# Kernel optimization log

Measured on AMD Instinct MI355X. Metric: run time of the kernel, lower is better.

The kernel has to match this reference:

```python
import jax, jax.numpy as jnp
import numpy as np

B, N1, N2, E = 128, 128, 384, 1024
N = N1 + N2
D_IN, D_FC = 64, 128
NUM_HEADS = 8.0  # args.num_att_heads
THETA = 1.0      # args.al_scale


def setup_inputs() -> dict:
    key = jax.random.key(0)
    ks = jax.random.split(key, 14)
    c_hs = jax.random.normal(ks[0], (B, N, D_IN), jnp.float32)
    attention = jax.random.uniform(ks[1], (B, N1, N2), jnp.float32)
    coords = jax.random.normal(ks[2], (B, N, 3), jnp.float32)
    upd_coords = coords + 0.1 * jax.random.normal(ks[3], (B, N, 3), jnp.float32)
    c_valid = jnp.ones((B, N), jnp.float32)
    nm = (jax.random.uniform(ks[4], (B, N1)) < 0.7).astype(jnp.float32)
    mapping = (jax.random.uniform(ks[5], (B, N, N)) < 0.05).astype(jnp.float32)
    samelb = jnp.maximum(mapping, (jax.random.uniform(ks[6], (B, N, N)) < 0.1).astype(jnp.float32))
    edge_index = jax.random.randint(ks[7], (B, E, 2), 0, N1, jnp.int32)
    W0 = jax.random.normal(ks[8], (D_IN, D_FC), jnp.float32) * 0.05
    b0 = jnp.zeros((D_FC,), jnp.float32)
    W1 = jax.random.normal(ks[9], (D_FC, D_FC), jnp.float32) * 0.05
    b1 = jnp.zeros((D_FC,), jnp.float32)
    W2 = jax.random.normal(ks[10], (D_FC, D_FC), jnp.float32) * 0.05
    b2 = jnp.zeros((D_FC,), jnp.float32)
    W3 = jax.random.normal(ks[11], (D_FC, 1), jnp.float32) * 0.05
    b3 = jnp.zeros((1,), jnp.float32)
    return dict(c_hs=c_hs, attention=attention, coords=coords, upd_coords=upd_coords,
                c_valid=c_valid, nm=nm, mapping=mapping, samelb=samelb,
                edge_index=edge_index, W0=W0, b0=b0, W1=W1, b1=b1, W2=W2, b2=b2, W3=W3, b3=b3)


def _kabsch(P, Q, m):
    # P, Q: [N1, 3], m: [N1] 0/1 non-modified mask
    Pm = P.mean(0)
    Qm = Q.mean(0)
    h = (P - Pm).T @ (Q - Qm) / NUM_HEADS  # [3,3]
    u, s, vt = jnp.linalg.svd(h)
    d = jnp.sign(jnp.linalg.det(h))
    corr = jnp.diag(jnp.concatenate([jnp.ones((2,), h.dtype), d[None].astype(h.dtype)]))
    r = u @ corr @ vt
    trans = Qm - r @ Pm
    Pp = P @ r.T + trans
    mk = (m > 0.5).astype(P.dtype)[:, None]
    cnt = jnp.maximum(mk.sum() * 3.0, 1.0)
    new_rmsd = (mk * (Pp - Q) ** 2).sum() / cnt        # mse over selected rows
    cen = ((Pp.mean(0) - Qm) ** 2).mean()              # centroid mse
    return new_rmsd, cen


def reference(c_hs, attention, coords, upd_coords, c_valid, nm, mapping, samelb,
              edge_index, W0, b0, W1, b1, W2, b2, W3, b3):
    # --- segment-sum pooling (sum_var_parts) + divide by n1, then FC head ---
    pooled = (c_hs * c_valid[..., None]).sum(axis=1) / float(N1)   # [B, D_IN]
    h = jax.nn.relu(pooled @ W0 + b0)
    h = jax.nn.relu(h @ W1 + b1)
    h = jax.nn.relu(h @ W2 + b2)
    scores = jax.nn.sigmoid(h @ W3 + b3).reshape(-1)               # [B]

    # --- cal_atten_batch + F.normalize(dim=1) ---
    atten = jnp.zeros((B, N, N), c_hs.dtype)
    atten = atten.at[:, :N1, N1:].set(attention)
    atten = atten.at[:, N1:, :N1].set(jnp.swapaxes(attention, 1, 2))
    nrm = jnp.sqrt((atten ** 2).sum(axis=1, keepdims=True))
    atten = atten / jnp.maximum(nrm, 1e-12)

    # --- cal_attn_loss ---
    top = jnp.where(mapping == 1.0, jnp.exp(-(atten * mapping)), 0.0).sum(axis=(1, 2))
    topabot = jnp.where(samelb == 1.0, jnp.exp(-(atten * samelb)), 0.0).sum(axis=(1, 2))
    attn_loss = (top / (topabot - top + 1.0)).sum() * THETA / float(B)

    # --- cal_rmsd_loss: straight-through one-hot mapping + Kabsch/SVD ---
    PP = upd_coords[:, :N1]   # subgraph updated coords
    QQ = coords[:, N1:]       # target graph original coords
    oh = jax.nn.one_hot(jnp.argmax(attention, axis=-1), N2, dtype=attention.dtype)
    st = oh + attention - jax.lax.stop_gradient(attention)         # straight-through
    Qsel = jnp.einsum('bij,bjd->bid', st, QQ)                      # [B, N1, 3]
    new_rmsd, cen = jax.vmap(_kabsch)(PP, Qsel, nm)
    rmsd_loss = new_rmsd.mean()
    centroid_loss = cen.mean()

    # --- cal_pairdst_loss over subgraph edges ---
    sub_c = coords[:, :N1]
    sub_u = upd_coords[:, :N1]
    bidx = jnp.arange(B)[:, None]
    d0 = jnp.sqrt(((sub_c[bidx, edge_index[..., 0]] - sub_c[bidx, edge_index[..., 1]]) ** 2).sum(-1) + 1e-12)
    d1 = jnp.sqrt(((sub_u[bidx, edge_index[..., 0]] - sub_u[bidx, edge_index[..., 1]]) ** 2).sum(-1) + 1e-12)
    pairdst_loss = jnp.abs((d1 - d0).sum(axis=-1)).mean()

    return scores, attn_loss, rmsd_loss, pairdst_loss, centroid_loss
```

## Files before the change

### kernel.cpp

```cpp
#include <hip/hip_runtime.h>
#include <math.h>

#define B_   128
#define N1_  128
#define N2_  384
#define N_   512
#define E_   1024
#define DIN  64
#define DFC  128

#define ACC_TOP  0
#define ACC_BOT  128
#define POOL_OFF 256
#define RNI_OFF  (POOL_OFF + B_*DIN)
#define CNI_OFF  (RNI_OFF + B_*N1_)
#define BI_OFF   (CNI_OFF + B_*N2_)
#define EB_OFF   (BI_OFF + B_*N1_)
#define ZERO_CNT (POOL_OFF + B_*DIN)

__global__ void k_init(float* ws, float* out) {
    int idx = blockIdx.x * 256 + threadIdx.x;
    if (idx < ZERO_CNT) ws[idx] = 0.f;
    if (blockIdx.x == 0 && threadIdx.x < 4) out[128 + threadIdx.x] = 0.f;
}

__global__ void k_pool(const float* __restrict__ c_hs, const float* __restrict__ c_valid,
                       float* __restrict__ ws) {
    __shared__ float4 sred[256];
    int b = blockIdx.x, t = threadIdx.x;
    int chunk = blockIdx.y * 64;
    int d4 = t & 15, rl = t >> 4;
    const float4* X4 = (const float4*)(c_hs + (size_t)b * N_ * DIN);
    const float* V = c_valid + (size_t)b * N_;
    float4 acc = {0.f, 0.f, 0.f, 0.f};
    #pragma unroll
    for (int r = chunk + rl; r < chunk + 64; r += 16) {
        float4 x = X4[r * 16 + d4];
        float v = V[r];
        acc.x += x.x * v; acc.y += x.y * v; acc.z += x.z * v; acc.w += x.w * v;
    }
    sred[t] = acc; __syncthreads();
    for (int off = 128; off >= 16; off >>= 1) {
        if (t < off) {
            float4 o = sred[t + off];
            sred[t].x += o.x; sred[t].y += o.y; sred[t].z += o.z; sred[t].w += o.w;
        }
        __syncthreads();
    }
    if (t < 16) {
        float4 s = sred[t];
        float* p = ws + POOL_OFF + b * DIN + t * 4;
        atomicAdd(&p[0], s.x); atomicAdd(&p[1], s.y);
        atomicAdd(&p[2], s.z); atomicAdd(&p[3], s.w);
    }
}

__global__ void k_mlp2(const float* __restrict__ ws,
                       const float* __restrict__ W0, const float* __restrict__ b0,
                       const float* __restrict__ W1, const float* __restrict__ b1,
                       const float* __restrict__ W2, const float* __restrict__ b2,
                       const float* __restrict__ W3, const float* __restrict__ b3,
                       float* __restrict__ out) {
    __shared__ float pool[DIN];
    __shared__ float h[DFC];
    __shared__ float h2[DFC];
    __shared__ float part[DFC];
    int b = blockIdx.x, t = threadIdx.x;
    if (t < DIN) pool[t] = ws[POOL_OFF + b * DIN + t] * (1.0f / 128.0f);
    __syncthreads();
    float a = b0[t];
    #pragma unroll
    for (int i = 0; i < DIN; ++i) a += pool[i] * W0[i * DFC + t];
    h[t] = fmaxf(a, 0.f); __syncthreads();
    a = b1[t];
    #pragma unroll
    for (int i = 0; i < DFC; ++i) a += h[i] * W1[i * DFC + t];
    h2[t] = fmaxf(a, 0.f); __syncthreads();
    a = b2[t];
    #pragma unroll
    for (int i = 0; i < DFC; ++i) a += h2[i] * W2[i * DFC + t];
    part[t] = fmaxf(a, 0.f) * W3[t];
    __syncthreads();
    for (int off = 64; off > 0; off >>= 1) { if (t < off) part[t] += part[t + off]; __syncthreads(); }
    if (t == 0) out[b] = 1.f / (1.f + expf(-(part[0] + b3[0])));
}

__global__ void k_rows(const float* __restrict__ att, float* __restrict__ ws) {
    int b = blockIdx.x, t = threadIdx.x, wv = t >> 6, ln = t & 63;
    int r = blockIdx.y * 4 + wv;
    const float* row = att + ((size_t)b * N1_ + r) * N2_;
    float ssq = 0.f, best = -1e30f; int bidx = 0;
    #pragma unroll
    for (int q = 0; q < 6; ++q) {
        float v = row[ln + 64 * q];
        ssq += v * v;
        if (v > best) { best = v; bidx = ln + 64 * q; }
    }
    for (int off = 32; off > 0; off >>= 1) {
        ssq += __shfl_xor(ssq, off, 64);
        float ov = __shfl_xor(best, off, 64);
        int oi = __shfl_xor(bidx, off, 64);
        if (ov > best || (ov == best && oi < bidx)) { best = ov; bidx = oi; }
    }
    if (ln == 0) {
        ws[RNI_OFF + b * N1_ + r] = 1.f / fmaxf(sqrtf(ssq), 1e-12f);
        ((int*)ws)[BI_OFF + b * N1_ + r] = bidx;
    }
}

__global__ void k_cols(const float* __restrict__ att, float* __restrict__ ws) {
    __shared__ float sred[256];
    int b = blockIdx.x, t = threadIdx.x;
    int c = blockIdx.y * 64 + (t & 63);
    int q = t >> 6;
    const float* A = att + (size_t)b * N1_ * N2_;
    float s = 0.f;
    #pragma unroll 8
    for (int j = q * 32; j < q * 32 + 32; ++j) { float v = A[j * N2_ + c]; s += v * v; }
    sred[t] = s; __syncthreads();
    if (t < 64)
        ws[CNI_OFF + b * N2_ + blockIdx.y * 64 + t] =
            1.f / fmaxf(sqrtf(sred[t] + sred[t + 64] + sred[t + 128] + sred[t + 192]), 1e-12f);
}

#define TP 129
__global__ void k_prep(const float* __restrict__ att, float* __restrict__ ws) {
    __shared__ float tile[32 * TP];
    __shared__ float rinv[N1_];
    int b = blockIdx.y, t = threadIdx.x;
    int r0 = blockIdx.x * 32;
    if (t < N1_) rinv[t] = ws[RNI_OFF + b * N1_ + t];
    __syncthreads();
    const float4* att4 = (const float4*)(att + (size_t)b * N1_ * N2_);
    int c8 = t & 7, jb = t >> 3;
    #pragma unroll
    for (int p = 0; p < 4; ++p) {
        int j = jb + p * 32;
        float4 a = att4[j * 96 + blockIdx.x * 8 + c8];
        float rv = rinv[j];
        tile[(c8 * 4 + 0) * TP + j] = a.x * rv;
        tile[(c8 * 4 + 1) * TP + j] = a.y * rv;
        tile[(c8 * 4 + 2) * TP + j] = a.z * rv;
        tile[(c8 * 4 + 3) * TP + j] = a.w * rv;
    }
    __syncthreads();
    int j4 = t & 31, cb = t >> 5;
    float4* eb4 = (float4*)(ws + EB_OFF + ((size_t)b * N2_ + r0) * N1_);
    #pragma unroll
    for (int p = 0; p < 4; ++p) {
        int c = cb + p * 8;
        float4 e;
        e.x = __expf(-tile[c * TP + j4 * 4]);
        e.y = __expf(-tile[c * TP + j4 * 4 + 1]);
        e.z = __expf(-tile[c * TP + j4 * 4 + 2]);
        e.w = __expf(-tile[c * TP + j4 * 4 + 3]);
        eb4[c * 32 + j4] = e;
    }
}

__global__ __launch_bounds__(256, 2)
void k_scan(const float* __restrict__ att, const float* __restrict__ mapping,
            const float* __restrict__ samelb, float* __restrict__ ws) {
    __shared__ float cninv[N2_];
    __shared__ float rt[4], rb[4];
    int b = blockIdx.y, t = threadIdx.x;
    int i0 = blockIdx.x * 16;
    const float4* m4 = (const float4*)(mapping + ((size_t)b * N_ + i0) * N_);
    const float4* s4 = (const float4*)(samelb + ((size_t)b * N_ + i0) * N_);
    float top = 0.f, bot = 0.f;
    if (i0 < N1_) {
        for (int j = t; j < N2_; j += 256) cninv[j] = ws[CNI_OFF + b * N2_ + j];
        __syncthreads();
        const float4* a4 = (const float4*)(att + ((size_t)b * N1_ + i0) * N2_);
        float4 md[2], sd[2], av[6], mv[6], sv[6];
        int ri[6], ci[6];
        #pragma unroll
        for (int k = 0; k < 2; ++k) { int g = t + k * 256; md[k] = m4[(g >> 5) * 128 + (g & 31)]; }
        #pragma unroll
        for (int k = 0; k < 2; ++k) { int g = t + k * 256; sd[k] = s4[(g >> 5) * 128 + (g & 31)]; }
        #pragma unroll
        for (int k = 0; k < 6; ++k) {
            int g = t + k * 256; ri[k] = g / 96; ci[k] = g - ri[k] * 96;
            av[k] = a4[ri[k] * 96 + ci[k]];
        }
        #pragma unroll
        for (int k = 0; k < 6; ++k) mv[k] = m4[ri[k] * 128 + 32 + ci[k]];
        #pragma unroll
        for (int k = 0; k < 6; ++k) sv[k] = s4[ri[k] * 128 + 32 + ci[k]];
        #pragma unroll
        for (int k = 0; k < 2; ++k) {
            top += md[k].x + md[k].y + md[k].z + md[k].w;
            bot += sd[k].x + sd[k].y + sd[k].z + sd[k].w;
        }
        #pragma unroll
        for (int k = 0; k < 6; ++k) {
            int cb = ci[k] * 4;
            float e0 = __expf(-av[k].x * cninv[cb]);
            float e1 = __expf(-av[k].y * cninv[cb + 1]);
            float e2 = __expf(-av[k].z * cninv[cb + 2]);
            float e3 = __expf(-av[k].w * cninv[cb + 3]);
            top += mv[k].x * e0 + mv[k].y * e1 + mv[k].z * e2 + mv[k].w * e3;
            bot += sv[k].x * e0 + sv[k].y * e1 + sv[k].z * e2 + sv[k].w * e3;
        }
    } else {
        const float4* eb4 = (const float4*)(ws + EB_OFF + ((size_t)b * N2_ + (i0 - N1_)) * N1_);
        float4 ev[2], mv[2], sv[2], mc[6], sc[6];
        #pragma unroll
        for (int k = 0; k < 2; ++k) { int g = t + k * 256; ev[k] = eb4[(g >> 5) * 32 + (g & 31)]; }
        #pragma unroll
        for (int k = 0; k < 2; ++k) { int g = t + k * 256; mv[k] = m4[(g >> 5) * 128 + (g & 31)]; }
        #pragma unroll
        for (int k = 0; k < 2; ++k) { int g = t + k * 256; sv[k] = s4[(g >> 5) * 128 + (g & 31)]; }
        #pragma unroll
        for (int k = 0; k < 6; ++k) {
            int g = t + k * 256; int r = g / 96, c = g - r * 96;
            mc[k] = m4[r * 128 + 32 + c];
        }
        #pragma unroll
        for (int k = 0; k < 6; ++k) {
            int g = t + k * 256; int r = g / 96, c = g - r * 96;
            sc[k] = s4[r * 128 + 32 + c];
        }
        #pragma unroll
        for (int k = 0; k < 2; ++k) {
            top += mv[k].x * ev[k].x + mv[k].y * ev[k].y + mv[k].z * ev[k].z + mv[k].w * ev[k].w;
            bot += sv[k].x * ev[k].x + sv[k].y * ev[k].y + sv[k].z * ev[k].z + sv[k].w * ev[k].w;
        }
        #pragma unroll
        for (int k = 0; k < 6; ++k) {
            top += mc[k].x + mc[k].y + mc[k].z + mc[k].w;
            bot += sc[k].x + sc[k].y + sc[k].z + sc[k].w;
        }
    }
    for (int off = 32; off > 0; off >>= 1) {
        top += __shfl_down(top, off, 64);
        bot += __shfl_down(bot, off, 64);
    }
    int wv = t >> 6, ln = t & 63;
    if (ln == 0) { rt[wv] = top; rb[wv] = bot; }
    __syncthreads();
    if (t == 0) {
        atomicAdd(&ws[ACC_TOP + b], rt[0] + rt[1] + rt[2] + rt[3]);
        atomicAdd(&ws[ACC_BOT + b], rb[0] + rb[1] + rb[2] + rb[3]);
    }
}

__device__ inline float bred(float* s2, float v, int t) {
    for (int off = 32; off > 0; off >>= 1) v += __shfl_down(v, off, 64);
    if ((t & 63) == 0) s2[t >> 6] = v;
    __syncthreads();
    float r = s2[0] + s2[1];
    __syncthreads();
    return r;
}

__global__ void k_kabsch(const float* __restrict__ coords, const float* __restrict__ upd,
                         const float* __restrict__ nm, const int* __restrict__ ei,
                         const float* __restrict__ ws, float* __restrict__ out) {
    __shared__ float s2[2];
    __shared__ float Rsh[9], Tsh[3];
    int b = blockIdx.x, t = threadIdx.x;
    int bidx = ((const int*)ws)[BI_OFF + b * N1_ + t];
    float P[3], Q[3];
    const float* up = upd + ((size_t)b * N_ + t) * 3;
    P[0] = up[0]; P[1] = up[1]; P[2] = up[2];
    const float* qp = coords + ((size_t)b * N_ + N1_ + bidx) * 3;
    Q[0] = qp[0]; Q[1] = qp[1]; Q[2] = qp[2];
    float Pm[3], Qm[3];
    for (int a = 0; a < 3; ++a) Pm[a] = bred(s2, P[a], t) * (1.f / 128.f);
    for (int a = 0; a < 3; ++a) Qm[a] = bred(s2, Q[a], t) * (1.f / 128.f);
    float H[9];
    for (int a = 0; a < 3; ++a)
        for (int c = 0; c < 3; ++c)
            H[a * 3 + c] = bred(s2, (P[a] - Pm[a]) * (Q[c] - Qm[c]), t) * (1.f / 8.f);
    if (t == 0) {
        double Hd[3][3];
        for (int a = 0; a < 3; ++a) for (int c = 0; c < 3; ++c) Hd[a][c] = (double)H[a * 3 + c];
        double A[3][3], V[3][3] = {{1,0,0},{0,1,0},{0,0,1}};
        for (int i = 0; i < 3; ++i)
            for (int j = 0; j < 3; ++j) {
                double z = 0; for (int c = 0; c < 3; ++c) z += Hd[c][i] * Hd[c][j];
                A[i][j] = z;
            }
        for (int sweep = 0; sweep < 8; ++sweep) {
            const int PQ[3][2] = {{0,1},{0,2},{1,2}};
            for (int r = 0; r < 3; ++r) {
                int p = PQ[r][0], q = PQ[r][1];
                double apq = A[p][q];
                if (fabs(apq) < 1e-300) continue;
                double tau = (A[q][q] - A[p][p]) / (2.0 * apq);
                double tt = (tau >= 0 ? 1.0 : -1.0) / (fabs(tau) + sqrt(1.0 + tau * tau));
                double c = 1.0 / sqrt(1.0 + tt * tt), s = tt * c;
                for (int k = 0; k < 3; ++k) { double akp = A[k][p], akq = A[k][q]; A[k][p] = c * akp - s * akq; A[k][q] = s * akp + c * akq; }
                for (int k = 0; k < 3; ++k) { double apk = A[p][k], aqk = A[q][k]; A[p][k] = c * apk - s * aqk; A[q][k] = s * apk + c * aqk; }
                for (int k = 0; k < 3; ++k) { double vkp = V[k][p], vkq = V[k][q]; V[k][p] = c * vkp - s * vkq; V[k][q] = s * vkp + c * vkq; }
            }
        }
        double lam[3] = {A[0][0], A[1][1], A[2][2]};
        int id[3] = {0, 1, 2};
        if (lam[id[0]] < lam[id[1]]) { int x = id[0]; id[0] = id[1]; id[1] = x; }
        if (lam[id[0]] < lam[id[2]]) { int x = id[0]; id[0] = id[2]; id[2] = x; }
        if (lam[id[1]] < lam[id[2]]) { int x = id[1]; id[1] = id[2]; id[2] = x; }
        double u[3][3], v[3][3], sv[3];
        for (int i = 0; i < 3; ++i) {
            for (int k = 0; k < 3; ++k) v[i][k] = V[k][id[i]];
            double uv[3];
            for (int c = 0; c < 3; ++c) uv[c] = Hd[c][0] * v[i][0] + Hd[c][1] * v[i][1] + Hd[c][2] * v[i][2];
            double n = sqrt(uv[0] * uv[0] + uv[1] * uv[1] + uv[2] * uv[2]);
            sv[i] = n;
            if (n > 1e-150) { u[i][0] = uv[0] / n; u[i][1] = uv[1] / n; u[i][2] = uv[2] / n; }
            else { u[i][0] = u[i][1] = u[i][2] = 0.0; }
        }
        if (sv[2] < 1e-12 * fmax(sv[0], 1e-300)) {
            u[2][0] = u[0][1] * u[1][2] - u[0][2] * u[1][1];
            u[2][1] = u[0][2] * u[1][0] - u[0][0] * u[1][2];
            u[2][2] = u[0][0] * u[1][1] - u[0][1] * u[1][0];
        }
        double det = Hd[0][0] * (Hd[1][1] * Hd[2][2] - Hd[1][2] * Hd[2][1])
                   - Hd[0][1] * (Hd[1][0] * Hd[2][2] - Hd[1][2] * Hd[2][0])
                   + Hd[0][2] * (Hd[1][0] * Hd[2][1] - Hd[1][1] * Hd[2][0]);
        double dsg = (det > 0.0) ? 1.0 : ((det < 0.0) ? -1.0 : 0.0);
        for (int a = 0; a < 3; ++a)
            for (int c = 0; c < 3; ++c)
                Rsh[a * 3 + c] = (float)(u[0][a] * v[0][c] + u[1][a] * v[1][c] + dsg * u[2][a] * v[2][c]);
        for (int a = 0; a < 3; ++a)
            Tsh[a] = Qm[a] - (Rsh[a * 3] * Pm[0] + Rsh[a * 3 + 1] * Pm[1] + Rsh[a * 3 + 2] * Pm[2]);
    }
    __syncthreads();
    float Pp[3];
    for (int a = 0; a < 3; ++a)
        Pp[a] = Rsh[a * 3] * P[0] + Rsh[a * 3 + 1] * P[1] + Rsh[a * 3 + 2] * P[2] + Tsh[a];
    float mk = (nm[b * N1_ + t] > 0.5f) ? 1.f : 0.f;
    float dx = Pp[0] - Q[0], dy = Pp[1] - Q[1], dz = Pp[2] - Q[2];
    float rsum = bred(s2, mk * (dx * dx + dy * dy + dz * dz), t);
    float msum = bred(s2, mk, t);
    float Ppm[3];
    for (int a = 0; a < 3; ++a) Ppm[a] = bred(s2, Pp[a], t) * (1.f / 128.f);
    if (t == 0) {
        float cnt = fmaxf(msum * 3.f, 1.f);
        atomicAdd(&out[129], (rsum / cnt) * (1.f / 128.f));
        float cen = 0.f;
        for (int a = 0; a < 3; ++a) { float d2 = Ppm[a] - Qm[a]; cen += d2 * d2; }
        atomicAdd(&out[131], (cen / 3.f) * (1.f / 128.f));
    }
    const float* C = coords + (size_t)b * N_ * 3;
    const float* U = upd + (size_t)b * N_ * 3;
    const int* e = ei + (size_t)b * E_ * 2;
    float acc = 0.f;
    for (int idx = t; idx < E_; idx += 128) {
        int a0 = e[idx * 2], a1 = e[idx * 2 + 1];
        float ex = C[a0 * 3] - C[a1 * 3], ey = C[a0 * 3 + 1] - C[a1 * 3 + 1], ez = C[a0 * 3 + 2] - C[a1 * 3 + 2];
        float d0 = sqrtf(ex * ex + ey * ey + ez * ez + 1e-12f);
        ex = U[a0 * 3] - U[a1 * 3]; ey = U[a0 * 3 + 1] - U[a1 * 3 + 1]; ez = U[a0 * 3 + 2] - U[a1 * 3 + 2];
        float d1 = sqrtf(ex * ex + ey * ey + ez * ez + 1e-12f);
        acc += d1 - d0;
    }
    float psum = bred(s2, acc, t);
    if (t == 0) atomicAdd(&out[130], fabsf(psum) * (1.f / 128.f));
    if (b == 0) {
        float top = ws[ACC_TOP + t], bot = ws[ACC_BOT + t];
        float v = top / (bot - top + 1.0f);
        float s = bred(s2, v, t);
        if (t == 0) out[128] = s * (1.0f / 128.0f);
    }
}

extern "C" void kernel_launch(void* const* d_in, const int* in_sizes, int n_in,
                              void* d_out, int out_size, void* d_ws, size_t ws_size,
                              hipStream_t stream) {
    const float* c_hs      = (const float*)d_in[0];
    const float* attention = (const float*)d_in[1];
    const float* coords    = (const float*)d_in[2];
    const float* upd       = (const float*)d_in[3];
    const float* c_valid   = (const float*)d_in[4];
    const float* nm        = (const float*)d_in[5];
    const float* mapping   = (const float*)d_in[6];
    const float* samelb    = (const float*)d_in[7];
    const int*   ei        = (const int*)d_in[8];
    const float* W0 = (const float*)d_in[9],  *b0 = (const float*)d_in[10];
    const float* W1 = (const float*)d_in[11], *b1 = (const float*)d_in[12];
    const float* W2 = (const float*)d_in[13], *b2 = (const float*)d_in[14];
    const float* W3 = (const float*)d_in[15], *b3 = (const float*)d_in[16];
    float* out = (float*)d_out;
    float* ws  = (float*)d_ws;

    hipLaunchKernelGGL(k_init,   dim3(33),      dim3(256), 0, stream, ws, out);
    hipLaunchKernelGGL(k_pool,   dim3(B_, 8),   dim3(256), 0, stream, c_hs, c_valid, ws);
    hipLaunchKernelGGL(k_mlp2,   dim3(B_),      dim3(DFC), 0, stream, ws,
                       W0, b0, W1, b1, W2, b2, W3, b3, out);
    hipLaunchKernelGGL(k_rows,   dim3(B_, 32),  dim3(256), 0, stream, attention, ws);
    hipLaunchKernelGGL(k_cols,   dim3(B_, 6),   dim3(256), 0, stream, attention, ws);
    hipLaunchKernelGGL(k_prep,   dim3(12, B_),  dim3(256), 0, stream, attention, ws);
    hipLaunchKernelGGL(k_scan,   dim3(32, B_),  dim3(256), 0, stream, attention, mapping, samelb, ws);
    hipLaunchKernelGGL(k_kabsch, dim3(B_),      dim3(N1_), 0, stream, coords, upd, nm, ei, ws, out);
}
```

Baseline: 387.6 us.

## Fuse pooling, row and column stats and MLP into fewer kernels, drop exp buffer

Merges pooling and the row-stat pass into one front kernel and accumulates column sums of squares there through shared atomics. A small finish kernel then converts those sums to inverse norms. The separate k_prep pass that wrote a transposed exp buffer to the workspace is gone: the scan kernel now computes the exp tile on the fly in shared memory. The MLP now runs as extra blocks of the Kabsch kernel. This cuts the launch count and the extra HBM round trip for the exp buffer, at the cost of global atomics for column sums, shared-memory atomics, and duplicated exp work.

```diff
diff --git a/kernel.cpp b/kernel.cpp
--- a/kernel.cpp
+++ b/kernel.cpp
@@ -13,89 +13,65 @@
 #define ACC_BOT  128
 #define POOL_OFF 256
 #define RNI_OFF  (POOL_OFF + B_*DIN)
-#define CNI_OFF  (RNI_OFF + B_*N1_)
-#define BI_OFF   (CNI_OFF + B_*N2_)
-#define EB_OFF   (BI_OFF + B_*N1_)
-#define ZERO_CNT (POOL_OFF + B_*DIN)
+#define BI_OFF   (RNI_OFF + B_*N1_)
+#define CNI_OFF  (BI_OFF + B_*N1_)
 
 __global__ void k_init(float* ws, float* out) {
     int idx = blockIdx.x * 256 + threadIdx.x;
-    if (idx < ZERO_CNT) ws[idx] = 0.f;
-    if (blockIdx.x == 0 && threadIdx.x < 4) out[128 + threadIdx.x] = 0.f;
-}
-
-__global__ void k_pool(const float* __restrict__ c_hs, const float* __restrict__ c_valid,
-                       float* __restrict__ ws) {
-    __shared__ float4 sred[256];
-    int b = blockIdx.x, t = threadIdx.x;
-    int chunk = blockIdx.y * 64;
-    int d4 = t & 15, rl = t >> 4;
-    const float4* X4 = (const float4*)(c_hs + (size_t)b * N_ * DIN);
-    const float* V = c_valid + (size_t)b * N_;
-    float4 acc = {0.f, 0.f, 0.f, 0.f};
-    #pragma unroll
-    for (int r = chunk + rl; r < chunk + 64; r += 16) {
-        float4 x = X4[r * 16 + d4];
-        float v = V[r];
-        acc.x += x.x * v; acc.y += x.y * v; acc.z += x.z * v; acc.w += x.w * v;
-    }
-    sred[t] = acc; __syncthreads();
-    for (int off = 128; off >= 16; off >>= 1) {
-        if (t < off) {
-            float4 o = sred[t + off];
-            sred[t].x += o.x; sred[t].y += o.y; sred[t].z += o.z; sred[t].w += o.w;
-        }
-        __syncthreads();
-    }
-    if (t < 16) {
-        float4 s = sred[t];
-        float* p = ws + POOL_OFF + b * DIN + t * 4;
-        atomicAdd(&p[0], s.x); atomicAdd(&p[1], s.y);
-        atomicAdd(&p[2], s.z); atomicAdd(&p[3], s.w);
-    }
-}
-
-__global__ void k_mlp2(const float* __restrict__ ws,
-                       const float* __restrict__ W0, const float* __restrict__ b0,
-                       const float* __restrict__ W1, const float* __restrict__ b1,
-                       const float* __restrict__ W2, const float* __restrict__ b2,
-                       const float* __restrict__ W3, const float* __restrict__ b3,
-                       float* __restrict__ out) {
-    __shared__ float pool[DIN];
-    __shared__ float h[DFC];
-    __shared__ float h2[DFC];
-    __shared__ float part[DFC];
-    int b = blockIdx.x, t = threadIdx.x;
-    if (t < DIN) pool[t] = ws[POOL_OFF + b * DIN + t] * (1.0f / 128.0f);
-    __syncthreads();
-    float a = b0[t];
-    #pragma unroll
-    for (int i = 0; i < DIN; ++i) a += pool[i] * W0[i * DFC + t];
-    h[t] = fmaxf(a, 0.f); __syncthreads();
-    a = b1[t];
-    #pragma unroll
-    for (int i = 0; i < DFC; ++i) a += h[i] * W1[i * DFC + t];
-    h2[t] = fmaxf(a, 0.f); __syncthreads();
-    a = b2[t];
-    #pragma unroll
-    for (int i = 0; i < DFC; ++i) a += h2[i] * W2[i * DFC + t];
-    part[t] = fmaxf(a, 0.f) * W3[t];
-    __syncthreads();
-    for (int off = 64; off > 0; off >>= 1) { if (t < off) part[t] += part[t + off]; __syncthreads(); }
-    if (t == 0) out[b] = 1.f / (1.f + expf(-(part[0] + b3[0])));
-}
-
-__global__ void k_rows(const float* __restrict__ att, float* __restrict__ ws) {
-    int b = blockIdx.x, t = threadIdx.x, wv = t >> 6, ln = t & 63;
-    int r = blockIdx.y * 4 + wv;
+    if (idx < 256 + B_ * DIN) ws[idx] = 0.f;
+    if (idx < B_ * N2_) ws[CNI_OFF + idx] = 0.f;
+    if (idx < 4) out[128 + idx] = 0.f;
+}
+
+__global__ void k_front(const float* __restrict__ c_hs, const float* __restrict__ c_valid,
+                        const float* __restrict__ att, float* __restrict__ ws) {
+    __shared__ float4 sred4[256];
+    int b = blockIdx.x, y = blockIdx.y, t = threadIdx.x;
+    if (y < 8) {
+        int chunk = y * 64;
+        int d4 = t & 15, rl = t >> 4;
+        const float4* X4 = (const float4*)(c_hs + (size_t)b * N_ * DIN);
+        const float* V = c_valid + (size_t)b * N_;
+        float4 acc = {0.f, 0.f, 0.f, 0.f};
+        #pragma unroll
+        for (int r = chunk + rl; r < chunk + 64; r += 16) {
+            float4 x = X4[r * 16 + d4];
+            float v = V[r];
+            acc.x += x.x * v; acc.y += x.y * v; acc.z += x.z * v; acc.w += x.w * v;
+        }
+        sred4[t] = acc; __syncthreads();
+        for (int off = 128; off >= 16; off >>= 1) {
+            if (t < off) {
+                float4 o = sred4[t + off];
+                sred4[t].x += o.x; sred4[t].y += o.y; sred4[t].z += o.z; sred4[t].w += o.w;
+            }
+            __syncthreads();
+        }
+        if (t < 16) {
+            float4 s = sred4[t];
+            float* p = ws + POOL_OFF + b * DIN + t * 4;
+            atomicAdd(&p[0], s.x); atomicAdd(&p[1], s.y);
+            atomicAdd(&p[2], s.z); atomicAdd(&p[3], s.w);
+        }
+        return;
+    }
+    float* colacc = (float*)sred4;
+    for (int c = t; c < N2_; c += 256) colacc[c] = 0.f;
+    __syncthreads();
+    int wv = t >> 6, ln = t & 63;
+    int r = (y - 8) * 4 + wv;
     const float* row = att + ((size_t)b * N1_ + r) * N2_;
+    float vv[6];
     float ssq = 0.f, best = -1e30f; int bidx = 0;
     #pragma unroll
     for (int q = 0; q < 6; ++q) {
         float v = row[ln + 64 * q];
+        vv[q] = v;
         ssq += v * v;
         if (v > best) { best = v; bidx = ln + 64 * q; }
     }
+    #pragma unroll
+    for (int q = 0; q < 6; ++q) atomicAdd(&colacc[ln + 64 * q], vv[q] * vv[q]);
     for (int off = 32; off > 0; off >>= 1) {
         ssq += __shfl_xor(ssq, off, 64);
         float ov = __shfl_xor(best, off, 64);
@@ -106,71 +82,32 @@
         ws[RNI_OFF + b * N1_ + r] = 1.f / fmaxf(sqrtf(ssq), 1e-12f);
         ((int*)ws)[BI_OFF + b * N1_ + r] = bidx;
     }
-}
-
-__global__ void k_cols(const float* __restrict__ att, float* __restrict__ ws) {
-    __shared__ float sred[256];
+    __syncthreads();
+    for (int c = t; c < N2_; c += 256)
+        atomicAdd(&ws[CNI_OFF + b * N2_ + c], colacc[c]);
+}
+
+__global__ void k_fin(float* __restrict__ ws) {
     int b = blockIdx.x, t = threadIdx.x;
-    int c = blockIdx.y * 64 + (t & 63);
-    int q = t >> 6;
-    const float* A = att + (size_t)b * N1_ * N2_;
-    float s = 0.f;
-    #pragma unroll 8
-    for (int j = q * 32; j < q * 32 + 32; ++j) { float v = A[j * N2_ + c]; s += v * v; }
-    sred[t] = s; __syncthreads();
-    if (t < 64)
-        ws[CNI_OFF + b * N2_ + blockIdx.y * 64 + t] =
-            1.f / fmaxf(sqrtf(sred[t] + sred[t + 64] + sred[t + 128] + sred[t + 192]), 1e-12f);
-}
-
-#define TP 129
-__global__ void k_prep(const float* __restrict__ att, float* __restrict__ ws) {
-    __shared__ float tile[32 * TP];
+    float v = ws[CNI_OFF + b * N2_ + t];
+    ws[CNI_OFF + b * N2_ + t] = 1.f / fmaxf(sqrtf(v), 1e-12f);
+}
+
+#define EWS 132
+__global__ void k_scan(const float* __restrict__ att, const float* __restrict__ mapping,
+                       const float* __restrict__ samelb, float* __restrict__ ws) {
+    __shared__ float cninv[N2_];
     __shared__ float rinv[N1_];
-    int b = blockIdx.y, t = threadIdx.x;
-    int r0 = blockIdx.x * 32;
-    if (t < N1_) rinv[t] = ws[RNI_OFF + b * N1_ + t];
-    __syncthreads();
-    const float4* att4 = (const float4*)(att + (size_t)b * N1_ * N2_);
-    int c8 = t & 7, jb = t >> 3;
-    #pragma unroll
-    for (int p = 0; p < 4; ++p) {
-        int j = jb + p * 32;
-        float4 a = att4[j * 96 + blockIdx.x * 8 + c8];
-        float rv = rinv[j];
-        tile[(c8 * 4 + 0) * TP + j] = a.x * rv;
-        tile[(c8 * 4 + 1) * TP + j] = a.y * rv;
-        tile[(c8 * 4 + 2) * TP + j] = a.z * rv;
-        tile[(c8 * 4 + 3) * TP + j] = a.w * rv;
-    }
-    __syncthreads();
-    int j4 = t & 31, cb = t >> 5;
-    float4* eb4 = (float4*)(ws + EB_OFF + ((size_t)b * N2_ + r0) * N1_);
-    #pragma unroll
-    for (int p = 0; p < 4; ++p) {
-        int c = cb + p * 8;
-        float4 e;
-        e.x = __expf(-tile[c * TP + j4 * 4]);
-        e.y = __expf(-tile[c * TP + j4 * 4 + 1]);
-        e.z = __expf(-tile[c * TP + j4 * 4 + 2]);
-        e.w = __expf(-tile[c * TP + j4 * 4 + 3]);
-        eb4[c * 32 + j4] = e;
-    }
-}
-
-__global__ __launch_bounds__(256, 2)
-void k_scan(const float* __restrict__ att, const float* __restrict__ mapping,
-            const float* __restrict__ samelb, float* __restrict__ ws) {
-    __shared__ float cninv[N2_];
+    __shared__ float ew[16 * EWS];
     __shared__ float rt[4], rb[4];
     int b = blockIdx.y, t = threadIdx.x;
-    int i0 = blockIdx.x * 16;
-    const float4* m4 = (const float4*)(mapping + ((size_t)b * N_ + i0) * N_);
-    const float4* s4 = (const float4*)(samelb + ((size_t)b * N_ + i0) * N_);
     float top = 0.f, bot = 0.f;
-    if (i0 < N1_) {
+    if (blockIdx.x < 8) {
+        int i0 = blockIdx.x * 16;
         for (int j = t; j < N2_; j += 256) cninv[j] = ws[CNI_OFF + b * N2_ + j];
         __syncthreads();
+        const float4* m4 = (const float4*)(mapping + ((size_t)b * N_ + i0) * N_);
+        const float4* s4 = (const float4*)(samelb + ((size_t)b * N_ + i0) * N_);
         const float4* a4 = (const float4*)(att + ((size_t)b * N1_ + i0) * N2_);
         float4 md[2], sd[2], av[6], mv[6], sv[6];
         int ri[6], ci[6];
@@ -203,10 +140,27 @@
             bot += sv[k].x * e0 + sv[k].y * e1 + sv[k].z * e2 + sv[k].w * e3;
         }
     } else {
-        const float4* eb4 = (const float4*)(ws + EB_OFF + ((size_t)b * N2_ + (i0 - N1_)) * N1_);
-        float4 ev[2], mv[2], sv[2], mc[6], sc[6];
-        #pragma unroll
-        for (int k = 0; k < 2; ++k) { int g = t + k * 256; ev[k] = eb4[(g >> 5) * 32 + (g & 31)]; }
+        int tb = blockIdx.x - 8;
+        int c0 = tb * 16;
+        int i0 = N1_ + c0;
+        if (t < N1_) rinv[t] = ws[RNI_OFF + b * N1_ + t];
+        __syncthreads();
+        const float4* att4 = (const float4*)(att + (size_t)b * N1_ * N2_);
+        int c4q = t & 3, jb = t >> 2;
+        #pragma unroll
+        for (int p = 0; p < 2; ++p) {
+            int j = jb + p * 64;
+            float4 a = att4[j * 96 + tb * 4 + c4q];
+            float rv = rinv[j];
+            ew[(c4q * 4 + 0) * EWS + j] = __expf(-a.x * rv);
+            ew[(c4q * 4 + 1) * EWS + j] = __expf(-a.y * rv);
+            ew[(c4q * 4 + 2) * EWS + j] = __expf(-a.z * rv);
+            ew[(c4q * 4 + 3) * EWS + j] = __expf(-a.w * rv);
+        }
+        __syncthreads();
+        const float4* m4 = (const float4*)(mapping + ((size_t)b * N_ + i0) * N_);
+        const float4* s4 = (const float4*)(samelb + ((size_t)b * N_ + i0) * N_);
+        float4 mv[2], sv[2], mc[6], sc[6];
         #pragma unroll
         for (int k = 0; k < 2; ++k) { int g = t + k * 256; mv[k] = m4[(g >> 5) * 128 + (g & 31)]; }
         #pragma unroll
@@ -223,8 +177,10 @@
         }
         #pragma unroll
         for (int k = 0; k < 2; ++k) {
-            top += mv[k].x * ev[k].x + mv[k].y * ev[k].y + mv[k].z * ev[k].z + mv[k].w * ev[k].w;
-            bot += sv[k].x * ev[k].x + sv[k].y * ev[k].y + sv[k].z * ev[k].z + sv[k].w * ev[k].w;
+            int g = t + k * 256; int r = g >> 5, c4 = g & 31;
+            float4 w = *(const float4*)&ew[r * EWS + c4 * 4];
+            top += mv[k].x * w.x + mv[k].y * w.y + mv[k].z * w.z + mv[k].w * w.w;
+            bot += sv[k].x * w.x + sv[k].y * w.y + sv[k].z * w.z + sv[k].w * w.w;
         }
         #pragma unroll
         for (int k = 0; k < 6; ++k) {
@@ -254,12 +210,42 @@
     return r;
 }
 
-__global__ void k_kabsch(const float* __restrict__ coords, const float* __restrict__ upd,
-                         const float* __restrict__ nm, const int* __restrict__ ei,
-                         const float* __restrict__ ws, float* __restrict__ out) {
-    __shared__ float s2[2];
+__global__ void k_back(const float* __restrict__ coords, const float* __restrict__ upd,
+                       const float* __restrict__ nm, const int* __restrict__ ei,
+                       const float* __restrict__ W0, const float* __restrict__ b0,
+                       const float* __restrict__ W1, const float* __restrict__ b1,
+                       const float* __restrict__ W2, const float* __restrict__ b2,
+                       const float* __restrict__ W3, const float* __restrict__ b3,
+                       const float* __restrict__ ws, float* __restrict__ out) {
+    __shared__ float sh[2 * DFC];
+    int b = blockIdx.x, t = threadIdx.x;
+    if (blockIdx.y == 1) {
+        float* pool = sh;
+        float* h    = sh + 64;
+        __shared__ float part[DFC];
+        if (t < DIN) pool[t] = ws[POOL_OFF + b * DIN + t] * (1.0f / 128.0f);
+        __syncthreads();
+        float a = b0[t];
+        #pragma unroll
+        for (int i = 0; i < DIN; ++i) a += pool[i] * W0[i * DFC + t];
+        float hv = fmaxf(a, 0.f);
+        __syncthreads(); h[t] = hv; __syncthreads();
+        a = b1[t];
+        #pragma unroll
+        for (int i = 0; i < DFC; ++i) a += h[i] * W1[i * DFC + t];
+        hv = fmaxf(a, 0.f);
+        __syncthreads(); h[t] = hv; __syncthreads();
+        a = b2[t];
+        #pragma unroll
+        for (int i = 0; i < DFC; ++i) a += h[i] * W2[i * DFC + t];
+        part[t] = fmaxf(a, 0.f) * W3[t];
+        __syncthreads();
+        for (int off = 64; off > 0; off >>= 1) { if (t < off) part[t] += part[t + off]; __syncthreads(); }
+        if (t == 0) out[b] = 1.f / (1.f + expf(-(part[0] + b3[0])));
+        return;
+    }
+    float* s2 = sh;
     __shared__ float Rsh[9], Tsh[3];
-    int b = blockIdx.x, t = threadIdx.x;
     int bidx = ((const int*)ws)[BI_OFF + b * N1_ + t];
     float P[3], Q[3];
     const float* up = upd + ((size_t)b * N_ + t) * 3;
@@ -384,13 +370,10 @@
     float* out = (float*)d_out;
     float* ws  = (float*)d_ws;
 
-    hipLaunchKernelGGL(k_init,   dim3(33),      dim3(256), 0, stream, ws, out);
-    hipLaunchKernelGGL(k_pool,   dim3(B_, 8),   dim3(256), 0, stream, c_hs, c_valid, ws);
-    hipLaunchKernelGGL(k_mlp2,   dim3(B_),      dim3(DFC), 0, stream, ws,
-                       W0, b0, W1, b1, W2, b2, W3, b3, out);
-    hipLaunchKernelGGL(k_rows,   dim3(B_, 32),  dim3(256), 0, stream, attention, ws);
-    hipLaunchKernelGGL(k_cols,   dim3(B_, 6),   dim3(256), 0, stream, attention, ws);
-    hipLaunchKernelGGL(k_prep,   dim3(12, B_),  dim3(256), 0, stream, attention, ws);
-    hipLaunchKernelGGL(k_scan,   dim3(32, B_),  dim3(256), 0, stream, attention, mapping, samelb, ws);
-    hipLaunchKernelGGL(k_kabsch, dim3(B_),      dim3(N1_), 0, stream, coords, upd, nm, ei, ws, out);
-}
+    hipLaunchKernelGGL(k_init,  dim3(192),     dim3(256), 0, stream, ws, out);
+    hipLaunchKernelGGL(k_front, dim3(B_, 40),  dim3(256), 0, stream, c_hs, c_valid, attention, ws);
+    hipLaunchKernelGGL(k_fin,   dim3(B_),      dim3(N2_), 0, stream, ws);
+    hipLaunchKernelGGL(k_scan,  dim3(32, B_),  dim3(256), 0, stream, attention, mapping, samelb, ws);
+    hipLaunchKernelGGL(k_back,  dim3(B_, 2),   dim3(128), 0, stream, coords, upd, nm, ei,
+                       W0, b0, W1, b1, W2, b2, W3, b3, ws, out);
+}
```

Measured after the change: 387.5 us. Within noise of the previous version (-0.0%).
